# Optimization experiments

Hardware: AMD Instinct MI355X
Metric: run time of the kernel (lower is better)

## Reference

```python
import jax, jax.numpy as jnp
import numpy as np

D_MODEL = 2048
NUM_HEADS = 16
HEAD_DIM = D_MODEL // NUM_HEADS
SCALE = HEAD_DIM ** 0.5
B, TQ, CACHE_LEN = 4, 1024, 1024


def setup_inputs() -> dict:
    key = jax.random.key(0)
    ks = jax.random.split(key, 13)
    f = jnp.float32
    inp = {
        'query': jax.random.normal(ks[0], (B, TQ, D_MODEL), f),
        'key': jax.random.normal(ks[1], (B, TQ, D_MODEL), f),
        'value': jax.random.normal(ks[2], (B, TQ, D_MODEL), f),
        'cache_key': jax.random.normal(ks[3], (B, CACHE_LEN, D_MODEL), f),
        'cache_value': jax.random.normal(ks[4], (B, CACHE_LEN, D_MODEL), f),
        'Wq': jax.random.normal(ks[5], (D_MODEL, D_MODEL), f) * 0.02,
        'bq': jnp.zeros((D_MODEL,), f),
        'Wk': jax.random.normal(ks[6], (D_MODEL, D_MODEL), f) * 0.02,
        'bk': jnp.zeros((D_MODEL,), f),
        'Wv': jax.random.normal(ks[7], (D_MODEL, D_MODEL), f) * 0.02,
        'bv': jnp.zeros((D_MODEL,), f),
        'Wo': jax.random.normal(ks[8], (D_MODEL, D_MODEL), f) * 0.02,
        'bo': jnp.zeros((D_MODEL,), f),
    }
    return inp


def _split(x):
    b, t, _ = x.shape
    return jnp.transpose(x.reshape(b, t, NUM_HEADS, HEAD_DIM), (0, 2, 1, 3))  # [B,H,T,Dh]


def reference(query, key, value, cache_key, cache_value, Wq, bq, Wk, bk, Wv, bv, Wo, bo):
    b, tq, _ = query.shape
    Q = query @ Wq.T + bq
    K = key @ Wk.T + bk
    V = value @ Wv.T + bv
    # cache holds already-projected K/V; concat along time
    K = jnp.concatenate([cache_key, K], axis=1)
    V = jnp.concatenate([cache_value, V], axis=1)
    total = K.shape[1]
    Qh, Kh, Vh = _split(Q), _split(K), _split(V)  # [B,H,T,Dh]
    scores = jnp.einsum('bhqd,bhkd->bhqk', Qh, Kh) / SCALE  # [B,H,Tq,total]
    # faithful to original: tril(Tq, total) mask (row i sees cols 0..i)
    mask = jnp.tril(jnp.ones((tq, total), dtype=bool))
    scores = jnp.where(mask[None, None], scores, -jnp.inf)
    attn = jax.nn.softmax(scores, axis=-1)  # eval mode: no dropout
    out = jnp.einsum('bhqk,bhkd->bhqd', attn, Vh)
    out = jnp.transpose(out, (0, 2, 1, 3)).reshape(b, tq, D_MODEL)
    out = out @ Wo.T + bo
    # new cache: torch reshapes the transposed [B,H,T,Dh] tensor directly
    new_k = Kh.reshape(b, -1, D_MODEL)
    new_v = Vh.reshape(b, -1, D_MODEL)
    return out, new_k, new_v
```

## Files before the change

kernel.cpp:

```cpp
#include <hip/hip_runtime.h>
#include <hip/hip_bf16.h>


typedef __bf16 bf16x8 __attribute__((ext_vector_type(8)));
typedef unsigned short u16x8 __attribute__((ext_vector_type(8)));
typedef float  f32x4  __attribute__((ext_vector_type(4)));
typedef unsigned int u32;

#define MFMA16(a, b, c) __builtin_amdgcn_mfma_f32_16x16x32_bf16((a), (b), (c), 0, 0, 0)

__device__ __forceinline__ void async16(__bf16* lds_p, const __bf16* g) {
    __builtin_amdgcn_global_load_lds(
        (__attribute__((address_space(1))) void*)g,
        (__attribute__((address_space(3))) void*)lds_p, 16, 0, 0);
}

__global__ __launch_bounds__(256) void prep(
    const float* __restrict__ q, const float* __restrict__ k, const float* __restrict__ v,
    const float* __restrict__ wq, const float* __restrict__ wk,
    const float* __restrict__ wv, const float* __restrict__ wo,
    const float* __restrict__ ck, const float* __restrict__ cv,
    float* __restrict__ nk, float* __restrict__ nv,
    __bf16* __restrict__ dq, __bf16* __restrict__ dk, __bf16* __restrict__ dv,
    __bf16* __restrict__ dwq, __bf16* __restrict__ dwk,
    __bf16* __restrict__ dwv, __bf16* __restrict__ dwo,
    __bf16* __restrict__ ckb, __bf16* __restrict__ cvb) {
    const int nthreads = gridDim.x * blockDim.x;
    for (int i = blockIdx.x * blockDim.x + threadIdx.x; i < 7340032; i += nthreads) {
        if (i < 2097152) {
            const int sel = i >> 20;
            const int j = i & 1048575;
            const int dh8 = j & 15;
            const int t = (j >> 4) & 1023;
            const int h = (j >> 14) & 15;
            const int b = j >> 18;
            const float* src = sel ? cv : ck;
            float* dst = sel ? nv : nk;
            __bf16* dstb = sel ? cvb : ckb;
            const size_t si = ((size_t)(b << 10) + t) * 2048 + (h << 7) + (dh8 << 3);
            const size_t di = ((size_t)b << 22) + ((size_t)h << 18) + (t << 7) + (dh8 << 3);
            const size_t bi = (((size_t)(b * 16 + h) * 1024 + t) << 7) + (dh8 << 3);
            const f32x4 x0 = *(const f32x4*)&src[si];
            const f32x4 x1 = *(const f32x4*)&src[si + 4];
            *(f32x4*)&dst[di] = x0;
            *(f32x4*)&dst[di + 4] = x1;
            bf16x8 bx;
#pragma unroll
            for (int e = 0; e < 4; e++) {
                bx[e]     = (__bf16)x0[e];
                bx[e + 4] = (__bf16)x1[e];
            }
            *(bf16x8*)&dstb[bi] = bx;
        } else {
            const float* s;
            __bf16* d;
            int off;
            if (i < 5242880) {
                const int ii = i - 2097152;
                const int r = ii >> 20;
                off = ii & 1048575;
                s = (r == 0) ? q : (r == 1) ? k : v;
                d = (r == 0) ? dq : (r == 1) ? dk : dv;
            } else {
                const int ii = i - 5242880;
                const int r = ii >> 19;
                off = ii & 524287;
                s = (r == 0) ? wq : (r == 1) ? wk : (r == 2) ? wv : wo;
                d = (r == 0) ? dwq : (r == 1) ? dwk : (r == 2) ? dwv : dwo;
            }
            const f32x4 x0 = *(const f32x4*)(s + (size_t)off * 8);
            const f32x4 x1 = *(const f32x4*)(s + (size_t)off * 8 + 4);
            bf16x8 o;
#pragma unroll
            for (int j2 = 0; j2 < 4; j2++) {
                o[j2]     = (__bf16)x0[j2];
                o[j2 + 4] = (__bf16)x1[j2];
            }
            *(bf16x8*)(d + (size_t)off * 8) = o;
        }
    }
}

template <int MODE>
__global__ __launch_bounds__(512, 2) void gemm8(
    const __bf16* __restrict__ A,
    const __bf16* __restrict__ W0, const __bf16* __restrict__ W1,
    const __bf16* __restrict__ W2,
    const float* __restrict__ bz0, const float* __restrict__ bz1,
    const float* __restrict__ bz2,
    void* __restrict__ C0, float* __restrict__ C1, float* __restrict__ C2) {
    extern __shared__ __bf16 lds[];
    constexpr int K = 2048;
    const int tid = threadIdx.x;
    const int w = tid >> 6, lane = tid & 63;
    const int wm = w >> 2, wn = w & 3;
    const int g = lane >> 4, c = lane & 15;

    const int lin = blockIdx.x;
    const int nb = lin & 7, mb = lin >> 3;
    const int m0 = mb << 7, n0 = nb << 8;
    const int seg = (MODE == 1) ? (mb >> 5) : 0;
    const __bf16* W = (MODE == 0 || seg == 0) ? W0 : (seg == 1) ? W1 : W2;
    const float* bias = (MODE == 0) ? bz0 : (seg == 0) ? bz0 : (seg == 1) ? bz1 : bz2;

    const __bf16* Ab = A + (size_t)m0 * K;
    const __bf16* Wb = W + (size_t)n0 * K;

    const int srow = lane >> 2;
    const int sch = (lane & 3) ^ (((lane >> 5) & 1) << 1);
    const int foff = c * 32 + ((g ^ ((c >> 3) << 1)) << 3);

    f32x4 acc[4][4] = {};

    auto stgA = [&](int T, int rg) {
#pragma unroll
        for (int u = 0; u < 2; u++) {
            const __bf16* gs = Ab + (size_t)(w * 16 + srow) * K + T * 64 + u * 32 + sch * 8;
            async16(&lds[rg * 24576 + (w * 2 + u) * 512], gs);
        }
    };
    auto stgB = [&](int T, int rg) {
#pragma unroll
        for (int u = 0; u < 4; u++) {
            const int rowblk = 2 * w + (u >> 1), kk = u & 1;
            const __bf16* gs = Wb + (size_t)(rowblk * 16 + srow) * K + T * 64 + kk * 32 + sch * 8;
            async16(&lds[rg * 24576 + 8192 + (w * 4 + u) * 512], gs);
        }
    };

    stgA(0, 0); stgB(0, 0);
    stgA(1, 1); stgB(1, 1);
    asm volatile("s_waitcnt vmcnt(6)" ::: "memory");
    asm volatile("s_barrier" ::: "memory");

    int rg = 0;
    for (int T = 0; T < 32; T++) {
        int rs = rg + 2; if (rs >= 3) rs -= 3;
        const int base = rg * 24576;
        bf16x8 fa[4], fb[4];

#pragma unroll
        for (int mi = 0; mi < 4; mi++)
            fa[mi] = *(const bf16x8*)&lds[base + ((wm * 4 + mi) * 2 + 0) * 512 + foff];
#pragma unroll
        for (int ni = 0; ni < 4; ni++)
            fb[ni] = *(const bf16x8*)&lds[base + 8192 + ((wn * 4 + ni) * 2 + 0) * 512 + foff];
        if (T < 30) stgA(T + 2, rs);
        asm volatile("s_barrier" ::: "memory");
        asm volatile("s_waitcnt lgkmcnt(0)" ::: "memory");
        __builtin_amdgcn_sched_barrier(0);
        __builtin_amdgcn_s_setprio(1);
#pragma unroll
        for (int mi = 0; mi < 4; mi++)
#pragma unroll
            for (int ni = 0; ni < 4; ni++)
                acc[mi][ni] = MFMA16(fa[mi], fb[ni], acc[mi][ni]);
        __builtin_amdgcn_s_setprio(0);
        asm volatile("s_barrier" ::: "memory");

#pragma unroll
        for (int mi = 0; mi < 4; mi++)
            fa[mi] = *(const bf16x8*)&lds[base + ((wm * 4 + mi) * 2 + 1) * 512 + foff];
#pragma unroll
        for (int ni = 0; ni < 4; ni++)
            fb[ni] = *(const bf16x8*)&lds[base + 8192 + ((wn * 4 + ni) * 2 + 1) * 512 + foff];
        if (T < 30) {
            stgB(T + 2, rs);
            asm volatile("s_waitcnt vmcnt(6)" ::: "memory");
        } else {
            asm volatile("s_waitcnt vmcnt(0)" ::: "memory");
        }
        asm volatile("s_barrier" ::: "memory");
        asm volatile("s_waitcnt lgkmcnt(0)" ::: "memory");
        __builtin_amdgcn_sched_barrier(0);
        __builtin_amdgcn_s_setprio(1);
#pragma unroll
        for (int mi = 0; mi < 4; mi++)
#pragma unroll
            for (int ni = 0; ni < 4; ni++)
                acc[mi][ni] = MFMA16(fa[mi], fb[ni], acc[mi][ni]);
        __builtin_amdgcn_s_setprio(0);
        asm volatile("s_barrier" ::: "memory");

        rg = (rg + 1 == 3) ? 0 : rg + 1;
    }

#pragma unroll
    for (int ni = 0; ni < 4; ni++) {
        const int col = n0 + wn * 64 + ni * 16 + c;
        const float bv = bias[col];
        const int h = col >> 7, dh = col & 127;
#pragma unroll
        for (int mi = 0; mi < 4; mi++) {
            const int rowb = m0 + wm * 64 + mi * 16 + g * 4;
#pragma unroll
            for (int r = 0; r < 4; r++) {
                const float v = acc[mi][ni][r] + bv;
                if (MODE == 0) {
                    ((float*)C0)[(size_t)(rowb + r) * 2048 + col] = v;
                } else {
                    const int lrow = (rowb + r) & 4095;
                    const int b = lrow >> 10, t = lrow & 1023;
                    if (seg == 0)
                        ((__bf16*)C0)[(((size_t)(b * 16 + h) * 1024) + t) * 128 + dh] = (__bf16)v;
                    else if (seg == 1)
                        C1[(((size_t)(b * 16 + h) * 2048) + 1024 + t) * 128 + dh] = v;
                    else
                        C2[(((size_t)(b * 16 + h) * 2048) + 1024 + t) * 128 + dh] = v;
                }
            }
        }
    }
}

__global__ __launch_bounds__(256) void attn_k(const __bf16* __restrict__ Qw,
                                              const __bf16* __restrict__ cK,
                                              const __bf16* __restrict__ cV,
                                              __bf16* __restrict__ O) {
    __shared__ __bf16 Kt[32 * 128];
    __shared__ u32 Vt32[128 * 16];
    __shared__ __bf16 Pw[4][16 * 32];

    const int tid = threadIdx.x;
    const int w = tid >> 6;
    const int lane = tid & 63;
    const int g = lane >> 4, c = lane & 15;

    const int lin = blockIdx.x + (blockIdx.y << 4) + (blockIdx.z << 8);
    const int chunk = lin >> 8, idx = lin & 255;
    int qb = idx & 15;
    if (chunk & 1) qb = 15 - qb;
    const int bh = (idx >> 4) + (chunk << 4);
    const int b = bh >> 4, h = bh & 15;
    const int q0 = qb << 6;
    const float inv_scale = 0.08838834764831845f;

    const __bf16* qbase = Qw + (((size_t)(b * 16 + h) * 1024) + q0 + w * 16) * 128;
    bf16x8 qf[4];
#pragma unroll
    for (int dc = 0; dc < 4; dc++)
        qf[dc] = *(const bf16x8*)&qbase[c * 128 + dc * 32 + g * 8];

    f32x4 accO[8] = {};
    float m_run[4], l_run[4];
#pragma unroll
    for (int r = 0; r < 4; r++) { m_run[r] = -1e30f; l_run[r] = 0.0f; }

    const int trips = (q0 >> 5) + 2;
    const __bf16* kb = cK + (size_t)(b * 16 + h) * 1024 * 128;
    const __bf16* vb = cV + (size_t)(b * 16 + h) * 1024 * 128;

    const int skey = tid >> 3, sdh = (tid & 7) * 16;
    const int kp = tid >> 4, db = tid & 15;
    const int vcol = (((kp >> 2) ^ (db & 3)) << 2) | (kp & 3);

    for (int kt = 0; kt < trips; kt++) {
        const int k0 = kt * 32;
        const bf16x8 k_lo = *(const bf16x8*)&kb[(size_t)(k0 + skey) * 128 + sdh];
        const bf16x8 k_hi = *(const bf16x8*)&kb[(size_t)(k0 + skey) * 128 + sdh + 8];
        const bf16x8 v0 = *(const bf16x8*)&vb[(size_t)(k0 + 2 * kp) * 128 + db * 8];
        const bf16x8 v1 = *(const bf16x8*)&vb[(size_t)(k0 + 2 * kp + 1) * 128 + db * 8];
        __syncthreads();
        {
            const int ss = skey & 7, ch0 = (tid & 7) * 2;
            *(bf16x8*)&Kt[skey * 128 + ((ch0 ^ ss) << 3)]       = k_lo;
            *(bf16x8*)&Kt[skey * 128 + (((ch0 + 1) ^ ss) << 3)] = k_hi;
        }
        {
            const u16x8 pa = __builtin_bit_cast(u16x8, v0);
            const u16x8 pb = __builtin_bit_cast(u16x8, v1);
#pragma unroll
            for (int j = 0; j < 8; j++)
                Vt32[(db * 8 + j) * 16 + vcol] = (u32)pa[j] | ((u32)pb[j] << 16);
        }
        __syncthreads();

        f32x4 s_acc[2] = {};
#pragma unroll
        for (int nt = 0; nt < 2; nt++) {
            const int krow = nt * 16 + c;
            const int ks = krow & 7;
#pragma unroll
            for (int dc = 0; dc < 4; dc++) {
                const bf16x8 kf =
                    *(const bf16x8*)&Kt[krow * 128 + (((dc * 4 + g) ^ ks) << 3)];
                s_acc[nt] = MFMA16(qf[dc], kf, s_acc[nt]);
            }
        }

        float p[2][4], alpha[4];
#pragma unroll
        for (int r = 0; r < 4; r++) {
            const int qrow = q0 + w * 16 + g * 4 + r;
            float s0 = (k0 + c      <= qrow) ? s_acc[0][r] * inv_scale : -1e30f;
            float s1 = (k0 + 16 + c <= qrow) ? s_acc[1][r] * inv_scale : -1e30f;
            float rm = fmaxf(s0, s1);
            rm = fmaxf(rm, __shfl_xor(rm, 1));
            rm = fmaxf(rm, __shfl_xor(rm, 2));
            rm = fmaxf(rm, __shfl_xor(rm, 4));
            rm = fmaxf(rm, __shfl_xor(rm, 8));
            const float mnew = fmaxf(m_run[r], rm);
            alpha[r] = __expf(m_run[r] - mnew);
            const float p0 = __expf(s0 - mnew);
            const float p1 = __expf(s1 - mnew);
            p[0][r] = p0; p[1][r] = p1;
            float ps = p0 + p1;
            ps += __shfl_xor(ps, 1);
            ps += __shfl_xor(ps, 2);
            ps += __shfl_xor(ps, 4);
            ps += __shfl_xor(ps, 8);
            l_run[r] = alpha[r] * l_run[r] + ps;
            m_run[r] = mnew;
        }
#pragma unroll
        for (int nt2 = 0; nt2 < 8; nt2++)
#pragma unroll
            for (int r = 0; r < 4; r++)
                accO[nt2][r] *= alpha[r];

#pragma unroll
        for (int nt = 0; nt < 2; nt++)
#pragma unroll
            for (int r = 0; r < 4; r++)
                Pw[w][(g * 4 + r) * 32 + ((((nt << 1) | (c >> 3)) ^ g) << 3) + (c & 7)] =
                    (__bf16)p[nt][r];
        asm volatile("s_waitcnt lgkmcnt(0)" ::: "memory");
        __builtin_amdgcn_sched_barrier(0);

        const bf16x8 pf = *(const bf16x8*)&Pw[w][c * 32 + ((g ^ ((c >> 2) & 3)) << 3)];
#pragma unroll
        for (int nt2 = 0; nt2 < 8; nt2++) {
            const int vrow = nt2 * 16 + c;
            const bf16x8 vf = *(const bf16x8*)&(
                (const __bf16*)Vt32)[vrow * 32 + ((g ^ ((vrow >> 3) & 3)) << 3)];
            accO[nt2] = MFMA16(pf, vf, accO[nt2]);
        }
    }

#pragma unroll
    for (int nt2 = 0; nt2 < 8; nt2++)
#pragma unroll
        for (int r = 0; r < 4; r++) {
            const float v = accO[nt2][r] / l_run[r];
            const int row = b * 1024 + q0 + w * 16 + g * 4 + r;
            const int col = h * 128 + nt2 * 16 + c;
            O[(size_t)row * 2048 + col] = (__bf16)v;
        }
}

extern "C" void kernel_launch(void* const* d_in, const int* in_sizes, int n_in,
                              void* d_out, int out_size, void* d_ws, size_t ws_size,
                              hipStream_t stream) {
    const float* query       = (const float*)d_in[0];
    const float* key         = (const float*)d_in[1];
    const float* value       = (const float*)d_in[2];
    const float* cache_key   = (const float*)d_in[3];
    const float* cache_value = (const float*)d_in[4];
    const float* Wq = (const float*)d_in[5];
    const float* bq = (const float*)d_in[6];
    const float* Wk = (const float*)d_in[7];
    const float* bk = (const float*)d_in[8];
    const float* Wv = (const float*)d_in[9];
    const float* bv = (const float*)d_in[10];
    const float* Wo = (const float*)d_in[11];
    const float* bo = (const float*)d_in[12];

    float* out   = (float*)d_out;
    float* new_k = out + 8388608;
    float* new_v = out + 25165824;

    __bf16* p = (__bf16*)d_ws;
    __bf16* ws_q    = p; p += 8388608;
    __bf16* ws_attn = p; p += 8388608;
    __bf16* q_bf    = p; p += 8388608;
    __bf16* k_bf    = p; p += 8388608;
    __bf16* v_bf    = p; p += 8388608;
    __bf16* wq_bf   = p; p += 4194304;
    __bf16* wk_bf   = p; p += 4194304;
    __bf16* wv_bf   = p; p += 4194304;
    __bf16* wo_bf   = p; p += 4194304;
    __bf16* ck_bf   = p; p += 8388608;
    __bf16* cv_bf   = p;

    static bool s_attr = false;
    if (!s_attr) {
        hipFuncSetAttribute(reinterpret_cast<const void*>(&gemm8<1>),
                            hipFuncAttributeMaxDynamicSharedMemorySize, 147456);
        hipFuncSetAttribute(reinterpret_cast<const void*>(&gemm8<0>),
                            hipFuncAttributeMaxDynamicSharedMemorySize, 147456);
        s_attr = true;
    }

    prep<<<4096, 256, 0, stream>>>(query, key, value, Wq, Wk, Wv, Wo,
                                   cache_key, cache_value, new_k, new_v,
                                   q_bf, k_bf, v_bf, wq_bf, wk_bf, wv_bf, wo_bf,
                                   ck_bf, cv_bf);
    gemm8<1><<<768, 512, 147456, stream>>>(q_bf, wq_bf, wk_bf, wv_bf,
                                           bq, bk, bv, ws_q, new_k, new_v);
    attn_k<<<dim3(16, 16, 4), 256, 0, stream>>>(ws_q, ck_bf, cv_bf, ws_attn);
    gemm8<0><<<256, 512, 147456, stream>>>(ws_attn, wo_bf, nullptr, nullptr,
                                           bo, nullptr, nullptr, out, nullptr, nullptr);
}
```

Before: 618.4 us.

## Replace 8-wave 128x256 GEMM tile with 2-wave 128x128 tile using static LDS

The projection GEMMs move from 512-thread blocks computing 128x256 tiles with K-step 64 to 128-thread blocks computing 128x128 tiles with K-step 32. Each wave now owns a 128x64 slice with 8x4 accumulators. LDS becomes a static 48KB triple buffer, and the dynamic-shared-memory attribute setup is dropped. The intent is more, smaller blocks for better CU occupancy and fewer barriers per MFMA. The cost is lower operand reuse per block, more global traffic and higher register pressure.

```diff
diff --git a/kernel.cpp b/kernel.cpp
--- a/kernel.cpp
+++ b/kernel.cpp
@@ -82,23 +82,23 @@
 }
 
 template <int MODE>
-__global__ __launch_bounds__(512, 2) void gemm8(
+__global__ __launch_bounds__(128, 2) void gemm2(
     const __bf16* __restrict__ A,
     const __bf16* __restrict__ W0, const __bf16* __restrict__ W1,
     const __bf16* __restrict__ W2,
     const float* __restrict__ bz0, const float* __restrict__ bz1,
     const float* __restrict__ bz2,
     void* __restrict__ C0, float* __restrict__ C1, float* __restrict__ C2) {
-    extern __shared__ __bf16 lds[];
     constexpr int K = 2048;
+    __shared__ __bf16 lds[3 * 8192];
+
     const int tid = threadIdx.x;
     const int w = tid >> 6, lane = tid & 63;
-    const int wm = w >> 2, wn = w & 3;
     const int g = lane >> 4, c = lane & 15;
 
     const int lin = blockIdx.x;
-    const int nb = lin & 7, mb = lin >> 3;
-    const int m0 = mb << 7, n0 = nb << 8;
+    const int nb = lin & 15, mb = lin >> 4;
+    const int m0 = mb << 7, n0 = nb << 7;
     const int seg = (MODE == 1) ? (mb >> 5) : 0;
     const __bf16* W = (MODE == 0 || seg == 0) ? W0 : (seg == 1) ? W1 : W2;
     const float* bias = (MODE == 0) ? bz0 : (seg == 0) ? bz0 : (seg == 1) ? bz1 : bz2;
@@ -110,89 +110,68 @@
     const int sch = (lane & 3) ^ (((lane >> 5) & 1) << 1);
     const int foff = c * 32 + ((g ^ ((c >> 3) << 1)) << 3);
 
-    f32x4 acc[4][4] = {};
-
-    auto stgA = [&](int T, int rg) {
-#pragma unroll
-        for (int u = 0; u < 2; u++) {
-            const __bf16* gs = Ab + (size_t)(w * 16 + srow) * K + T * 64 + u * 32 + sch * 8;
-            async16(&lds[rg * 24576 + (w * 2 + u) * 512], gs);
+    f32x4 acc[8][4] = {};
+
+    auto stg = [&](int T, int rg) {
+        const int kof = T * 32 + sch * 8;
+#pragma unroll
+        for (int s = 0; s < 4; s++) {
+            const int st = w * 4 + s;
+            async16(&lds[rg * 8192 + st * 512],
+                    Ab + (size_t)(st * 16 + srow) * K + kof);
+        }
+#pragma unroll
+        for (int s = 0; s < 4; s++) {
+            const int st = w * 4 + s;
+            async16(&lds[rg * 8192 + 4096 + st * 512],
+                    Wb + (size_t)(st * 16 + srow) * K + kof);
         }
     };
-    auto stgB = [&](int T, int rg) {
-#pragma unroll
-        for (int u = 0; u < 4; u++) {
-            const int rowblk = 2 * w + (u >> 1), kk = u & 1;
-            const __bf16* gs = Wb + (size_t)(rowblk * 16 + srow) * K + T * 64 + kk * 32 + sch * 8;
-            async16(&lds[rg * 24576 + 8192 + (w * 4 + u) * 512], gs);
-        }
-    };
-
-    stgA(0, 0); stgB(0, 0);
-    stgA(1, 1); stgB(1, 1);
-    asm volatile("s_waitcnt vmcnt(6)" ::: "memory");
-    asm volatile("s_barrier" ::: "memory");
-
-    int rg = 0;
-    for (int T = 0; T < 32; T++) {
-        int rs = rg + 2; if (rs >= 3) rs -= 3;
-        const int base = rg * 24576;
-        bf16x8 fa[4], fb[4];
-
-#pragma unroll
-        for (int mi = 0; mi < 4; mi++)
-            fa[mi] = *(const bf16x8*)&lds[base + ((wm * 4 + mi) * 2 + 0) * 512 + foff];
+
+    stg(0, 0);
+    stg(1, 1);
+    asm volatile("s_waitcnt vmcnt(8)" ::: "memory");
+    __builtin_amdgcn_s_barrier();
+
+    int rg = 0, rs = 2;
+    for (int T = 0; T < 64; T++) {
+        const int base = rg * 8192;
+        bf16x8 fa[8], fb[4];
+#pragma unroll
+        for (int mi = 0; mi < 8; mi++)
+            fa[mi] = *(const bf16x8*)&lds[base + mi * 512 + foff];
 #pragma unroll
         for (int ni = 0; ni < 4; ni++)
-            fb[ni] = *(const bf16x8*)&lds[base + 8192 + ((wn * 4 + ni) * 2 + 0) * 512 + foff];
-        if (T < 30) stgA(T + 2, rs);
-        asm volatile("s_barrier" ::: "memory");
+            fb[ni] = *(const bf16x8*)&lds[base + 4096 + (w * 4 + ni) * 512 + foff];
+        if (T <= 61) {
+            stg(T + 2, rs);
+            asm volatile("s_waitcnt vmcnt(8)" ::: "memory");
+        } else {
+            asm volatile("s_waitcnt vmcnt(0)" ::: "memory");
+        }
+        __builtin_amdgcn_s_barrier();
         asm volatile("s_waitcnt lgkmcnt(0)" ::: "memory");
         __builtin_amdgcn_sched_barrier(0);
         __builtin_amdgcn_s_setprio(1);
 #pragma unroll
-        for (int mi = 0; mi < 4; mi++)
+        for (int mi = 0; mi < 8; mi++)
 #pragma unroll
             for (int ni = 0; ni < 4; ni++)
                 acc[mi][ni] = MFMA16(fa[mi], fb[ni], acc[mi][ni]);
         __builtin_amdgcn_s_setprio(0);
-        asm volatile("s_barrier" ::: "memory");
-
-#pragma unroll
-        for (int mi = 0; mi < 4; mi++)
-            fa[mi] = *(const bf16x8*)&lds[base + ((wm * 4 + mi) * 2 + 1) * 512 + foff];
-#pragma unroll
-        for (int ni = 0; ni < 4; ni++)
-            fb[ni] = *(const bf16x8*)&lds[base + 8192 + ((wn * 4 + ni) * 2 + 1) * 512 + foff];
-        if (T < 30) {
-            stgB(T + 2, rs);
-            asm volatile("s_waitcnt vmcnt(6)" ::: "memory");
-        } else {
-            asm volatile("s_waitcnt vmcnt(0)" ::: "memory");
-        }
-        asm volatile("s_barrier" ::: "memory");
-        asm volatile("s_waitcnt lgkmcnt(0)" ::: "memory");
-        __builtin_amdgcn_sched_barrier(0);
-        __builtin_amdgcn_s_setprio(1);
-#pragma unroll
-        for (int mi = 0; mi < 4; mi++)
-#pragma unroll
-            for (int ni = 0; ni < 4; ni++)
-                acc[mi][ni] = MFMA16(fa[mi], fb[ni], acc[mi][ni]);
-        __builtin_amdgcn_s_setprio(0);
-        asm volatile("s_barrier" ::: "memory");
-
-        rg = (rg + 1 == 3) ? 0 : rg + 1;
+        __builtin_amdgcn_s_barrier();
+        rg = (rg == 2) ? 0 : rg + 1;
+        rs = (rs == 2) ? 0 : rs + 1;
     }
 
 #pragma unroll
     for (int ni = 0; ni < 4; ni++) {
-        const int col = n0 + wn * 64 + ni * 16 + c;
+        const int col = n0 + w * 64 + ni * 16 + c;
         const float bv = bias[col];
         const int h = col >> 7, dh = col & 127;
 #pragma unroll
-        for (int mi = 0; mi < 4; mi++) {
-            const int rowb = m0 + wm * 64 + mi * 16 + g * 4;
+        for (int mi = 0; mi < 8; mi++) {
+            const int rowb = m0 + mi * 16 + g * 4;
 #pragma unroll
             for (int r = 0; r < 4; r++) {
                 const float v = acc[mi][ni][r] + bv;
@@ -382,22 +361,13 @@
     __bf16* ck_bf   = p; p += 8388608;
     __bf16* cv_bf   = p;
 
-    static bool s_attr = false;
-    if (!s_attr) {
-        hipFuncSetAttribute(reinterpret_cast<const void*>(&gemm8<1>),
-                            hipFuncAttributeMaxDynamicSharedMemorySize, 147456);
-        hipFuncSetAttribute(reinterpret_cast<const void*>(&gemm8<0>),
-                            hipFuncAttributeMaxDynamicSharedMemorySize, 147456);
-        s_attr = true;
-    }
-
     prep<<<4096, 256, 0, stream>>>(query, key, value, Wq, Wk, Wv, Wo,
                                    cache_key, cache_value, new_k, new_v,
                                    q_bf, k_bf, v_bf, wq_bf, wk_bf, wv_bf, wo_bf,
                                    ck_bf, cv_bf);
-    gemm8<1><<<768, 512, 147456, stream>>>(q_bf, wq_bf, wk_bf, wv_bf,
-                                           bq, bk, bv, ws_q, new_k, new_v);
+    gemm2<1><<<1536, 128, 0, stream>>>(q_bf, wq_bf, wk_bf, wv_bf,
+                                       bq, bk, bv, ws_q, new_k, new_v);
     attn_k<<<dim3(16, 16, 4), 256, 0, stream>>>(ws_q, ck_bf, cv_bf, ws_attn);
-    gemm8<0><<<256, 512, 147456, stream>>>(ws_attn, wo_bf, nullptr, nullptr,
-                                           bo, nullptr, nullptr, out, nullptr, nullptr);
-}
+    gemm2<0><<<512, 128, 0, stream>>>(ws_attn, wo_bf, nullptr, nullptr,
+                                      bo, nullptr, nullptr, out, nullptr, nullptr);
+}
```

After: 637.5 us. 3.1% more time.

## Double key tile to 64, prefetch next K/V into registers, remap blocks per XCD

Applied to the files above, without the earlier changes.

The attention kernel now processes 64 keys per iteration instead of 32, which halves the number of barrier-separated trips. It issues the global loads for the next tile into registers right after the LDS barrier, so memory latency overlaps with the MFMA and softmax work. Block indices are remapped so each XCD handles a contiguous group of batch-heads, with a balanced causal query-block ordering. In exchange, LDS use and register pressure go up, and a launch bound of 4 blocks per SM is requested.

```diff
diff --git a/kernel.cpp b/kernel.cpp
--- a/kernel.cpp
+++ b/kernel.cpp
@@ -213,13 +213,13 @@
     }
 }
 
-__global__ __launch_bounds__(256) void attn_k(const __bf16* __restrict__ Qw,
-                                              const __bf16* __restrict__ cK,
-                                              const __bf16* __restrict__ cV,
-                                              __bf16* __restrict__ O) {
-    __shared__ __bf16 Kt[32 * 128];
-    __shared__ u32 Vt32[128 * 16];
-    __shared__ __bf16 Pw[4][16 * 32];
+__global__ __launch_bounds__(256, 4) void attn_k(const __bf16* __restrict__ Qw,
+                                                 const __bf16* __restrict__ cK,
+                                                 const __bf16* __restrict__ cV,
+                                                 __bf16* __restrict__ O) {
+    __shared__ __bf16 Kt[64 * 128];
+    __shared__ u32    Vt32[128 * 32];
+    __shared__ __bf16 Pw[4][16 * 64];
 
     const int tid = threadIdx.x;
     const int w = tid >> 6;
@@ -227,15 +227,16 @@
     const int g = lane >> 4, c = lane & 15;
 
     const int lin = blockIdx.x + (blockIdx.y << 4) + (blockIdx.z << 8);
-    const int chunk = lin >> 8, idx = lin & 255;
-    int qb = idx & 15;
-    if (chunk & 1) qb = 15 - qb;
-    const int bh = (idx >> 4) + (chunk << 4);
-    const int b = bh >> 4, h = bh & 15;
+    const int xcd = lin & 7;
+    const int j = lin >> 3;
+    const int rr = j >> 5, s = j & 31;
+    const int bh = xcd * 8 + (s >> 2);
+    const int kq = s & 3;
+    const int qb = (rr == 0) ? kq : (rr == 1) ? 15 - kq : (rr == 2) ? 7 - kq : 8 + kq;
     const int q0 = qb << 6;
     const float inv_scale = 0.08838834764831845f;
 
-    const __bf16* qbase = Qw + (((size_t)(b * 16 + h) * 1024) + q0 + w * 16) * 128;
+    const __bf16* qbase = Qw + (((size_t)bh * 1024) + q0 + w * 16) * 128;
     bf16x8 qf[4];
 #pragma unroll
     for (int dc = 0; dc < 4; dc++)
@@ -246,38 +247,54 @@
 #pragma unroll
     for (int r = 0; r < 4; r++) { m_run[r] = -1e30f; l_run[r] = 0.0f; }
 
-    const int trips = (q0 >> 5) + 2;
-    const __bf16* kb = cK + (size_t)(b * 16 + h) * 1024 * 128;
-    const __bf16* vb = cV + (size_t)(b * 16 + h) * 1024 * 128;
+    const int trips = qb + 1;
+    const __bf16* kb = cK + (size_t)bh * 1024 * 128;
+    const __bf16* vb = cV + (size_t)bh * 1024 * 128;
 
     const int skey = tid >> 3, sdh = (tid & 7) * 16;
+    const int ss = skey & 7, ch0 = (tid & 7) * 2;
     const int kp = tid >> 4, db = tid & 15;
-    const int vcol = (((kp >> 2) ^ (db & 3)) << 2) | (kp & 3);
+    const int vlc = ((kp >> 2) ^ (db & 3));
+
+    bf16x8 kreg[2][2], vreg[2][2];
+    auto load_regs = [&](int k0) {
+#pragma unroll
+        for (int hh = 0; hh < 2; hh++) {
+            const __bf16* kr = kb + (size_t)(k0 + hh * 32 + skey) * 128 + sdh;
+            kreg[hh][0] = *(const bf16x8*)&kr[0];
+            kreg[hh][1] = *(const bf16x8*)&kr[8];
+            const __bf16* vr = vb + (size_t)(k0 + hh * 32 + 2 * kp) * 128 + db * 8;
+            vreg[hh][0] = *(const bf16x8*)&vr[0];
+            vreg[hh][1] = *(const bf16x8*)&vr[128];
+        }
+    };
+
+    load_regs(0);
 
     for (int kt = 0; kt < trips; kt++) {
-        const int k0 = kt * 32;
-        const bf16x8 k_lo = *(const bf16x8*)&kb[(size_t)(k0 + skey) * 128 + sdh];
-        const bf16x8 k_hi = *(const bf16x8*)&kb[(size_t)(k0 + skey) * 128 + sdh + 8];
-        const bf16x8 v0 = *(const bf16x8*)&vb[(size_t)(k0 + 2 * kp) * 128 + db * 8];
-        const bf16x8 v1 = *(const bf16x8*)&vb[(size_t)(k0 + 2 * kp + 1) * 128 + db * 8];
+        const int k0 = kt * 64;
         __syncthreads();
-        {
-            const int ss = skey & 7, ch0 = (tid & 7) * 2;
-            *(bf16x8*)&Kt[skey * 128 + ((ch0 ^ ss) << 3)]       = k_lo;
-            *(bf16x8*)&Kt[skey * 128 + (((ch0 + 1) ^ ss) << 3)] = k_hi;
-        }
-        {
-            const u16x8 pa = __builtin_bit_cast(u16x8, v0);
-            const u16x8 pb = __builtin_bit_cast(u16x8, v1);
-#pragma unroll
-            for (int j = 0; j < 8; j++)
-                Vt32[(db * 8 + j) * 16 + vcol] = (u32)pa[j] | ((u32)pb[j] << 16);
+#pragma unroll
+        for (int hh = 0; hh < 2; hh++) {
+            const int row = hh * 32 + skey;
+            *(bf16x8*)&Kt[row * 128 + ((ch0 ^ ss) << 3)]       = kreg[hh][0];
+            *(bf16x8*)&Kt[row * 128 + (((ch0 + 1) ^ ss) << 3)] = kreg[hh][1];
+            const u16x8 pa = __builtin_bit_cast(u16x8, vreg[hh][0]);
+            const u16x8 pb = __builtin_bit_cast(u16x8, vreg[hh][1]);
+            const int lc = hh * 4 + vlc;
+#pragma unroll
+            for (int jj = 0; jj < 8; jj++) {
+                const int d = db * 8 + jj;
+                Vt32[d * 32 + ((lc ^ jj) << 2) + (kp & 3)] =
+                    (u32)pa[jj] | ((u32)pb[jj] << 16);
+            }
         }
         __syncthreads();
-
-        f32x4 s_acc[2] = {};
-#pragma unroll
-        for (int nt = 0; nt < 2; nt++) {
+        if (kt + 1 < trips) load_regs(k0 + 64);
+
+        f32x4 s_acc[4] = {};
+#pragma unroll
+        for (int nt = 0; nt < 4; nt++) {
             const int krow = nt * 16 + c;
             const int ks = krow & 7;
 #pragma unroll
@@ -288,23 +305,27 @@
             }
         }
 
-        float p[2][4], alpha[4];
+        float p[4][4], alpha[4];
 #pragma unroll
         for (int r = 0; r < 4; r++) {
             const int qrow = q0 + w * 16 + g * 4 + r;
-            float s0 = (k0 + c      <= qrow) ? s_acc[0][r] * inv_scale : -1e30f;
-            float s1 = (k0 + 16 + c <= qrow) ? s_acc[1][r] * inv_scale : -1e30f;
-            float rm = fmaxf(s0, s1);
+            float sv[4];
+#pragma unroll
+            for (int nt = 0; nt < 4; nt++)
+                sv[nt] = (k0 + nt * 16 + c <= qrow) ? s_acc[nt][r] * inv_scale : -1e30f;
+            float rm = fmaxf(fmaxf(sv[0], sv[1]), fmaxf(sv[2], sv[3]));
             rm = fmaxf(rm, __shfl_xor(rm, 1));
             rm = fmaxf(rm, __shfl_xor(rm, 2));
             rm = fmaxf(rm, __shfl_xor(rm, 4));
             rm = fmaxf(rm, __shfl_xor(rm, 8));
             const float mnew = fmaxf(m_run[r], rm);
             alpha[r] = __expf(m_run[r] - mnew);
-            const float p0 = __expf(s0 - mnew);
-            const float p1 = __expf(s1 - mnew);
-            p[0][r] = p0; p[1][r] = p1;
-            float ps = p0 + p1;
+            float ps = 0.0f;
+#pragma unroll
+            for (int nt = 0; nt < 4; nt++) {
+                p[nt][r] = __expf(sv[nt] - mnew);
+                ps += p[nt][r];
+            }
             ps += __shfl_xor(ps, 1);
             ps += __shfl_xor(ps, 2);
             ps += __shfl_xor(ps, 4);
@@ -319,21 +340,30 @@
                 accO[nt2][r] *= alpha[r];
 
 #pragma unroll
-        for (int nt = 0; nt < 2; nt++)
-#pragma unroll
-            for (int r = 0; r < 4; r++)
-                Pw[w][(g * 4 + r) * 32 + ((((nt << 1) | (c >> 3)) ^ g) << 3) + (c & 7)] =
-                    (__bf16)p[nt][r];
+        for (int nt = 0; nt < 4; nt++)
+#pragma unroll
+            for (int r = 0; r < 4; r++) {
+                const int row = g * 4 + r;
+                const int cc = (nt * 2 + (c >> 3)) ^ (row & 7);
+                Pw[w][row * 64 + (cc << 3) + (c & 7)] = (__bf16)p[nt][r];
+            }
         asm volatile("s_waitcnt lgkmcnt(0)" ::: "memory");
         __builtin_amdgcn_sched_barrier(0);
 
-        const bf16x8 pf = *(const bf16x8*)&Pw[w][c * 32 + ((g ^ ((c >> 2) & 3)) << 3)];
+        bf16x8 pf[2];
+#pragma unroll
+        for (int s2 = 0; s2 < 2; s2++)
+            pf[s2] = *(const bf16x8*)&Pw[w][c * 64 + (((s2 * 4 + g) ^ (c & 7)) << 3)];
 #pragma unroll
         for (int nt2 = 0; nt2 < 8; nt2++) {
-            const int vrow = nt2 * 16 + c;
-            const bf16x8 vf = *(const bf16x8*)&(
-                (const __bf16*)Vt32)[vrow * 32 + ((g ^ ((vrow >> 3) & 3)) << 3)];
-            accO[nt2] = MFMA16(pf, vf, accO[nt2]);
+            const int d = nt2 * 16 + c;
+#pragma unroll
+            for (int s2 = 0; s2 < 2; s2++) {
+                const int lc = s2 * 4 + (g ^ ((d >> 3) & 3));
+                const bf16x8 vf = *(const bf16x8*)&(
+                    (const __bf16*)Vt32)[d * 64 + ((lc ^ (d & 7)) << 3)];
+                accO[nt2] = MFMA16(pf[s2], vf, accO[nt2]);
+            }
         }
     }
 
@@ -342,8 +372,8 @@
 #pragma unroll
         for (int r = 0; r < 4; r++) {
             const float v = accO[nt2][r] / l_run[r];
-            const int row = b * 1024 + q0 + w * 16 + g * 4 + r;
-            const int col = h * 128 + nt2 * 16 + c;
+            const int row = (bh >> 4) * 1024 + q0 + w * 16 + g * 4 + r;
+            const int col = (bh & 15) * 128 + nt2 * 16 + c;
             O[(size_t)row * 2048 + col] = (__bf16)v;
         }
 }
```

New measurement: 716.9 us. 15.9% more time.

## Halve attention query tile to 32 rows with XCD-aware block mapping

Applied to the files above, without the earlier changes.

The attention kernel now uses 128-thread blocks, each covering 32 query rows with two waves instead of 64 rows with four, and launches twice as many blocks. A new block-index mapping groups heads by XCD (lin & 7) so blocks sharing K/V land on the same L2, and pairs long and short causal tiles for load balance. Each thread loads twice as much K/V per tile to fill the shared-memory staging. The aim is finer granularity and better causal-work balance across CUs, at the cost of K/V tiles being reloaded by more blocks.

```diff
diff --git a/kernel.cpp b/kernel.cpp
--- a/kernel.cpp
+++ b/kernel.cpp
@@ -213,13 +213,13 @@
     }
 }
 
-__global__ __launch_bounds__(256) void attn_k(const __bf16* __restrict__ Qw,
+__global__ __launch_bounds__(128) void attn_k(const __bf16* __restrict__ Qw,
                                               const __bf16* __restrict__ cK,
                                               const __bf16* __restrict__ cV,
                                               __bf16* __restrict__ O) {
     __shared__ __bf16 Kt[32 * 128];
     __shared__ u32 Vt32[128 * 16];
-    __shared__ __bf16 Pw[4][16 * 32];
+    __shared__ __bf16 Pw[2][16 * 32];
 
     const int tid = threadIdx.x;
     const int w = tid >> 6;
@@ -227,15 +227,17 @@
     const int g = lane >> 4, c = lane & 15;
 
     const int lin = blockIdx.x + (blockIdx.y << 4) + (blockIdx.z << 8);
-    const int chunk = lin >> 8, idx = lin & 255;
-    int qb = idx & 15;
-    if (chunk & 1) qb = 15 - qb;
-    const int bh = (idx >> 4) + (chunk << 4);
+    const int xcd = lin & 7;
+    const int j = lin >> 3;
+    const int bh = xcd * 8 + (j & 7);
+    const int qq = j >> 3;
+    const int c4 = qq & 3, m = qq >> 2;
+    const int qb = ((m & 1) == 0) ? (c4 * 4 + (m >> 1)) : (31 - c4 * 4 - (m >> 1));
     const int b = bh >> 4, h = bh & 15;
-    const int q0 = qb << 6;
+    const int q0 = qb << 5;
     const float inv_scale = 0.08838834764831845f;
 
-    const __bf16* qbase = Qw + (((size_t)(b * 16 + h) * 1024) + q0 + w * 16) * 128;
+    const __bf16* qbase = Qw + (((size_t)bh * 1024) + q0 + w * 16) * 128;
     bf16x8 qf[4];
 #pragma unroll
     for (int dc = 0; dc < 4; dc++)
@@ -246,32 +248,49 @@
 #pragma unroll
     for (int r = 0; r < 4; r++) { m_run[r] = -1e30f; l_run[r] = 0.0f; }
 
-    const int trips = (q0 >> 5) + 2;
-    const __bf16* kb = cK + (size_t)(b * 16 + h) * 1024 * 128;
-    const __bf16* vb = cV + (size_t)(b * 16 + h) * 1024 * 128;
-
-    const int skey = tid >> 3, sdh = (tid & 7) * 16;
-    const int kp = tid >> 4, db = tid & 15;
-    const int vcol = (((kp >> 2) ^ (db & 3)) << 2) | (kp & 3);
+    const int trips = qb + 1;
+    const __bf16* kb = cK + (size_t)bh * 1024 * 128;
+    const __bf16* vb = cV + (size_t)bh * 1024 * 128;
+
+    const int skey = tid >> 2, sgrp = tid & 3;
+    const int ss = skey & 7;
+    const int kp = tid >> 3, dbv = tid & 7;
 
     for (int kt = 0; kt < trips; kt++) {
         const int k0 = kt * 32;
-        const bf16x8 k_lo = *(const bf16x8*)&kb[(size_t)(k0 + skey) * 128 + sdh];
-        const bf16x8 k_hi = *(const bf16x8*)&kb[(size_t)(k0 + skey) * 128 + sdh + 8];
-        const bf16x8 v0 = *(const bf16x8*)&vb[(size_t)(k0 + 2 * kp) * 128 + db * 8];
-        const bf16x8 v1 = *(const bf16x8*)&vb[(size_t)(k0 + 2 * kp + 1) * 128 + db * 8];
+        const __bf16* kr = &kb[(size_t)(k0 + skey) * 128 + sgrp * 32];
+        const bf16x8 k_a = *(const bf16x8*)&kr[0];
+        const bf16x8 k_b = *(const bf16x8*)&kr[8];
+        const bf16x8 k_c = *(const bf16x8*)&kr[16];
+        const bf16x8 k_d = *(const bf16x8*)&kr[24];
+        const __bf16* vr0 = &vb[(size_t)(k0 + 2 * kp) * 128 + dbv * 16];
+        const __bf16* vr1 = &vb[(size_t)(k0 + 2 * kp + 1) * 128 + dbv * 16];
+        const bf16x8 v0a = *(const bf16x8*)&vr0[0];
+        const bf16x8 v0b = *(const bf16x8*)&vr0[8];
+        const bf16x8 v1a = *(const bf16x8*)&vr1[0];
+        const bf16x8 v1b = *(const bf16x8*)&vr1[8];
         __syncthreads();
         {
-            const int ss = skey & 7, ch0 = (tid & 7) * 2;
-            *(bf16x8*)&Kt[skey * 128 + ((ch0 ^ ss) << 3)]       = k_lo;
-            *(bf16x8*)&Kt[skey * 128 + (((ch0 + 1) ^ ss) << 3)] = k_hi;
+            const int c0 = sgrp * 4;
+            *(bf16x8*)&Kt[skey * 128 + (((c0 + 0) ^ ss) << 3)] = k_a;
+            *(bf16x8*)&Kt[skey * 128 + (((c0 + 1) ^ ss) << 3)] = k_b;
+            *(bf16x8*)&Kt[skey * 128 + (((c0 + 2) ^ ss) << 3)] = k_c;
+            *(bf16x8*)&Kt[skey * 128 + (((c0 + 3) ^ ss) << 3)] = k_d;
         }
         {
-            const u16x8 pa = __builtin_bit_cast(u16x8, v0);
-            const u16x8 pb = __builtin_bit_cast(u16x8, v1);
-#pragma unroll
-            for (int j = 0; j < 8; j++)
-                Vt32[(db * 8 + j) * 16 + vcol] = (u32)pa[j] | ((u32)pb[j] << 16);
+            const u16x8 a0 = __builtin_bit_cast(u16x8, v0a);
+            const u16x8 a1 = __builtin_bit_cast(u16x8, v0b);
+            const u16x8 b0 = __builtin_bit_cast(u16x8, v1a);
+            const u16x8 b1 = __builtin_bit_cast(u16x8, v1b);
+#pragma unroll
+            for (int jj = 0; jj < 8; jj++) {
+                const int d0 = dbv * 16 + jj;
+                const int d1 = dbv * 16 + 8 + jj;
+                const int pc0 = (((kp >> 2) ^ ((d0 >> 3) & 3)) << 2) | (kp & 3);
+                const int pc1 = (((kp >> 2) ^ ((d1 >> 3) & 3)) << 2) | (kp & 3);
+                Vt32[d0 * 16 + pc0] = (u32)a0[jj] | ((u32)b0[jj] << 16);
+                Vt32[d1 * 16 + pc1] = (u32)a1[jj] | ((u32)b1[jj] << 16);
+            }
         }
         __syncthreads();
 
@@ -397,7 +416,7 @@
                                    ck_bf, cv_bf);
     gemm8<1><<<768, 512, 147456, stream>>>(q_bf, wq_bf, wk_bf, wv_bf,
                                            bq, bk, bv, ws_q, new_k, new_v);
-    attn_k<<<dim3(16, 16, 4), 256, 0, stream>>>(ws_q, ck_bf, cv_bf, ws_attn);
+    attn_k<<<dim3(16, 16, 8), 128, 0, stream>>>(ws_q, ck_bf, cv_bf, ws_attn);
     gemm8<0><<<256, 512, 147456, stream>>>(ws_attn, wo_bf, nullptr, nullptr,
                                            bo, nullptr, nullptr, out, nullptr, nullptr);
 }
```

New measurement: 617.9 us (median of 2 runs). About the same (-0.1%).
